# Optimization experiments

Hardware: AMD Instinct MI355X
Metric: run time of the kernel (lower is better)

## Reference

```python
import jax, jax.numpy as jnp
import numpy as np

NUM_HEADS = 16
ROPE_THETA = 10000.0


def _rope_angles(seq_len, head_dim, dtype):
    # lucidrains rotary_embedding_torch: freqs = theta^(-2i/d) for i in 0..d/2,
    # angles = pos * freq, then each angle repeated twice along last dim (interleaved pairs).
    inv_freq = 1.0 / (ROPE_THETA ** (jnp.arange(0, head_dim, 2, dtype=jnp.float32) / head_dim))
    angles = jnp.arange(seq_len, dtype=jnp.float32)[:, None] * inv_freq  # [N, D/2]
    return jnp.repeat(angles, 2, axis=-1).astype(dtype)  # [N, D]


def _rotate_half(t):
    # interleaved pairs: (x0, x1) -> (-x1, x0)
    t1 = t[..., ::2]
    t2 = t[..., 1::2]
    return jnp.stack([-t2, t1], axis=-1).reshape(t.shape)


def _apply_rope(t, cos, sin):
    # t: [B, H, N, D]; cos/sin: [N, D]
    return t * cos + _rotate_half(t) * sin


def setup_inputs() -> dict:
    key = jax.random.key(0)
    ks = jax.random.split(key, 5)
    B, N, C = 4, 1024, 1024
    return {
        "x": jax.random.normal(ks[0], (B, N, C), dtype=jnp.float32),
        "w_qkv": jax.random.normal(ks[1], (C, 3 * C), dtype=jnp.float32) * (C ** -0.5),
        "b_qkv": jax.random.normal(ks[2], (3 * C,), dtype=jnp.float32) * 0.02,
        "w_proj": jax.random.normal(ks[3], (C, C), dtype=jnp.float32) * (C ** -0.5),
        "b_proj": jax.random.normal(ks[4], (C,), dtype=jnp.float32) * 0.02,
    }


def reference(x, w_qkv, b_qkv, w_proj, b_proj):
    B, N, C = x.shape
    H = NUM_HEADS
    D = C // H

    qkv = x @ w_qkv + b_qkv  # [B, N, 3C]
    qkv = qkv.reshape(B, N, 3, H, D).transpose(2, 0, 3, 1, 4)  # [3, B, H, N, D]
    q, k, v = qkv[0], qkv[1], qkv[2]

    ang = _rope_angles(N, D, x.dtype)
    cos, sin = jnp.cos(ang), jnp.sin(ang)
    q = _apply_rope(q, cos, sin)
    k = _apply_rope(k, cos, sin)

    scale = D ** -0.5  # SDPA default scale
    scores = jnp.einsum("bhqd,bhkd->bhqk", q, k) * scale
    attn = jax.nn.softmax(scores, axis=-1)
    out = jnp.einsum("bhqk,bhkd->bhqd", attn, v)  # [B, H, N, D]

    out = out.transpose(0, 2, 1, 3).reshape(B, N, C)
    return out @ w_proj + b_proj
```

## Files before the change

### kernel.cpp

```cpp
#include <hip/hip_runtime.h>
#include <math.h>

#define BB 4
#define NN 1024
#define CC 1024
#define HH 16
#define DD 64
#define N3 3072

typedef __attribute__((ext_vector_type(8))) short bf16x8;
typedef __attribute__((ext_vector_type(8))) _Float16 f16x8;
typedef __attribute__((ext_vector_type(4))) _Float16 f16x4;
typedef __attribute__((ext_vector_type(4))) float f32x4;
typedef __attribute__((ext_vector_type(4))) unsigned int u32x4;

struct ushort4_t { unsigned short x, y, z, w; };

static __device__ __forceinline__ unsigned short f2b(float f) {
    union { float f; unsigned int u; } v; v.f = f;
    unsigned int r = (v.u + 0x7fffu + ((v.u >> 16) & 1u)) >> 16;
    return (unsigned short)r;
}

static __device__ __forceinline__ void ldg_lds16(const void* g, void* l) {
    __builtin_amdgcn_global_load_lds(
        (const __attribute__((address_space(1))) unsigned int*)g,
        (__attribute__((address_space(3))) unsigned int*)l, 16, 0, 0);
}

__global__ __launch_bounds__(256) void prep(const float* __restrict__ x,
                                            const float* __restrict__ wq,
                                            const float* __restrict__ wp,
                                            _Float16* __restrict__ Xh,
                                            _Float16* __restrict__ Wqt,
                                            _Float16* __restrict__ Wpt,
                                            float* __restrict__ ct,
                                            float* __restrict__ st) {
    const int blk = blockIdx.x;
    const int t = threadIdx.x;
    if (blk < 4096) {
        int tid = blk * 256 + t;
        float4 v = ((const float4*)x)[tid];
        f16x4 o = {(_Float16)v.x, (_Float16)v.y, (_Float16)v.z, (_Float16)v.w};
        ((f16x4*)Xh)[tid] = o;
    } else if (blk < 5632) {
        int idx = blk - 4096;
        int n  = (idx % 12) * 256 + t;
        int k0 = (idx / 12) * 8;
        f16x8 o;
        #pragma unroll
        for (int kk = 0; kk < 8; kk++)
            o[kk] = (_Float16)wq[(size_t)(k0 + kk) * N3 + n];
        *(f16x8*)(Wqt + (size_t)n * 1024 + k0) = o;
    } else if (blk < 6144) {
        int idx = blk - 5632;
        int n  = (idx % 4) * 256 + t;
        int k0 = (idx / 4) * 8;
        f16x8 o;
        #pragma unroll
        for (int kk = 0; kk < 8; kk++)
            o[kk] = (_Float16)wp[(size_t)(k0 + kk) * 1024 + n];
        *(f16x8*)(Wpt + (size_t)n * 1024 + k0) = o;
    } else {
        int tid = (blk - 6144) * 256 + t;
        int n = tid >> 5, i = tid & 31;
        double ang = (double)n * exp2(-(double)i * (13.287712379549449 / 32.0));
        ct[tid] = (float)cos(ang);
        st[tid] = (float)sin(ang);
    }
}

static __device__ __forceinline__ void gemm_body_pipe(const char* gA, const char* gB,
                                                      int m0, int n0,
                                                      _Float16* As0, _Float16* As1,
                                                      _Float16* Bs0, _Float16* Bs1,
                                                      int tid, int ln, int qd,
                                                      int wm, int wn, f32x4 acc[4][4]) {
    const int lrow   = tid >> 3;
    const int lchunk = tid & 7;
    const int swz    = (lchunk ^ (lrow & 7)) * 8;

    u32x4 pa[4], pb[4];

    #pragma unroll
    for (int c = 0; c < 4; c++) {
        size_t ra = (size_t)(m0 + c * 32 + lrow) * 2048 + lchunk * 16;
        size_t rb = (size_t)(n0 + c * 32 + lrow) * 2048 + lchunk * 16;
        pa[c] = *(const u32x4*)(gA + ra);
        pb[c] = *(const u32x4*)(gB + rb);
    }
    #pragma unroll
    for (int c = 0; c < 4; c++) {
        *(u32x4*)&As0[(c * 32 + lrow) * 64 + swz] = pa[c];
        *(u32x4*)&Bs0[(c * 32 + lrow) * 64 + swz] = pb[c];
    }
    #pragma unroll
    for (int c = 0; c < 4; c++) {
        size_t ra = (size_t)(m0 + c * 32 + lrow) * 2048 + 128 + lchunk * 16;
        size_t rb = (size_t)(n0 + c * 32 + lrow) * 2048 + 128 + lchunk * 16;
        pa[c] = *(const u32x4*)(gA + ra);
        pb[c] = *(const u32x4*)(gB + rb);
    }
    __syncthreads();

    #pragma unroll
    for (int t = 0; t < 16; t++) {
        const _Float16* Ac = (t & 1) ? As1 : As0;
        const _Float16* Bc = (t & 1) ? Bs1 : Bs0;

        #pragma unroll
        for (int kc = 0; kc < 2; kc++) {
            f16x8 af[4], bf[4];
            #pragma unroll
            for (int i = 0; i < 4; i++)
                af[i] = *(const f16x8*)&Ac[(wm + i * 16 + ln) * 64 +
                                           (((kc * 4 + qd) ^ (ln & 7)) * 8)];
            #pragma unroll
            for (int j = 0; j < 4; j++)
                bf[j] = *(const f16x8*)&Bc[(wn + j * 16 + ln) * 64 +
                                           (((kc * 4 + qd) ^ (ln & 7)) * 8)];
            #pragma unroll
            for (int i = 0; i < 4; i++)
                #pragma unroll
                for (int j = 0; j < 4; j++)
                    acc[i][j] = __builtin_amdgcn_mfma_f32_16x16x32_f16(af[i], bf[j],
                                                                       acc[i][j], 0, 0, 0);
        }

        if (t < 15) {
            _Float16* An = (t & 1) ? As0 : As1;
            _Float16* Bn = (t & 1) ? Bs0 : Bs1;
            #pragma unroll
            for (int c = 0; c < 4; c++) {
                *(u32x4*)&An[(c * 32 + lrow) * 64 + swz] = pa[c];
                *(u32x4*)&Bn[(c * 32 + lrow) * 64 + swz] = pb[c];
            }
            if (t < 14) {
                size_t ko = (size_t)(t + 2) * 128;
                #pragma unroll
                for (int c = 0; c < 4; c++) {
                    size_t ra = (size_t)(m0 + c * 32 + lrow) * 2048 + ko + lchunk * 16;
                    size_t rb = (size_t)(n0 + c * 32 + lrow) * 2048 + ko + lchunk * 16;
                    pa[c] = *(const u32x4*)(gA + ra);
                    pb[c] = *(const u32x4*)(gB + rb);
                }
            }
        }
        __syncthreads();
    }
}

static __device__ __forceinline__ void gemm_body_pipe_n64(const char* gA, const char* gB,
                                                          int m0, int n0,
                                                          _Float16* As0, _Float16* As1,
                                                          _Float16* Bs0, _Float16* Bs1,
                                                          int tid, int ln, int qd,
                                                          int wm, int wn, f32x4 acc[4][2]) {
    const int lrow   = tid >> 3;
    const int lchunk = tid & 7;
    const int swz    = (lchunk ^ (lrow & 7)) * 8;

    u32x4 pa[4], pb[2];

    #pragma unroll
    for (int c = 0; c < 4; c++)
        pa[c] = *(const u32x4*)(gA + (size_t)(m0 + c * 32 + lrow) * 2048 + lchunk * 16);
    #pragma unroll
    for (int c = 0; c < 2; c++)
        pb[c] = *(const u32x4*)(gB + (size_t)(n0 + c * 32 + lrow) * 2048 + lchunk * 16);
    #pragma unroll
    for (int c = 0; c < 4; c++)
        *(u32x4*)&As0[(c * 32 + lrow) * 64 + swz] = pa[c];
    #pragma unroll
    for (int c = 0; c < 2; c++)
        *(u32x4*)&Bs0[(c * 32 + lrow) * 64 + swz] = pb[c];
    #pragma unroll
    for (int c = 0; c < 4; c++)
        pa[c] = *(const u32x4*)(gA + (size_t)(m0 + c * 32 + lrow) * 2048 + 128 + lchunk * 16);
    #pragma unroll
    for (int c = 0; c < 2; c++)
        pb[c] = *(const u32x4*)(gB + (size_t)(n0 + c * 32 + lrow) * 2048 + 128 + lchunk * 16);
    __syncthreads();

    #pragma unroll
    for (int t = 0; t < 16; t++) {
        const _Float16* Ac = (t & 1) ? As1 : As0;
        const _Float16* Bc = (t & 1) ? Bs1 : Bs0;

        #pragma unroll
        for (int kc = 0; kc < 2; kc++) {
            f16x8 af[4], bf[2];
            #pragma unroll
            for (int i = 0; i < 4; i++)
                af[i] = *(const f16x8*)&Ac[(wm + i * 16 + ln) * 64 +
                                           (((kc * 4 + qd) ^ (ln & 7)) * 8)];
            #pragma unroll
            for (int j = 0; j < 2; j++)
                bf[j] = *(const f16x8*)&Bc[(wn + j * 16 + ln) * 64 +
                                           (((kc * 4 + qd) ^ (ln & 7)) * 8)];
            #pragma unroll
            for (int i = 0; i < 4; i++)
                #pragma unroll
                for (int j = 0; j < 2; j++)
                    acc[i][j] = __builtin_amdgcn_mfma_f32_16x16x32_f16(af[i], bf[j],
                                                                       acc[i][j], 0, 0, 0);
        }

        if (t < 15) {
            _Float16* An = (t & 1) ? As0 : As1;
            _Float16* Bn = (t & 1) ? Bs0 : Bs1;
            #pragma unroll
            for (int c = 0; c < 4; c++)
                *(u32x4*)&An[(c * 32 + lrow) * 64 + swz] = pa[c];
            #pragma unroll
            for (int c = 0; c < 2; c++)
                *(u32x4*)&Bn[(c * 32 + lrow) * 64 + swz] = pb[c];
            if (t < 14) {
                size_t ko = (size_t)(t + 2) * 128;
                #pragma unroll
                for (int c = 0; c < 4; c++)
                    pa[c] = *(const u32x4*)(gA + (size_t)(m0 + c * 32 + lrow) * 2048 + ko + lchunk * 16);
                #pragma unroll
                for (int c = 0; c < 2; c++)
                    pb[c] = *(const u32x4*)(gB + (size_t)(n0 + c * 32 + lrow) * 2048 + ko + lchunk * 16);
            }
        }
        __syncthreads();
    }
}

__global__ __launch_bounds__(256) void qkv_mfma(const _Float16* __restrict__ Ah,
                                                const _Float16* __restrict__ Bt,
                                                const float* __restrict__ bias,
                                                const float* __restrict__ cost,
                                                const float* __restrict__ sint,
                                                unsigned short* __restrict__ Q,
                                                unsigned short* __restrict__ K,
                                                unsigned short* __restrict__ Vtg) {
    __shared__ __align__(16) _Float16 As[2][128 * 64];
    __shared__ __align__(16) _Float16 Bs[2][128 * 64];
    const int t = threadIdx.x;
    const int lane = t & 63;
    const int w = t >> 6;
    const int ln = lane & 15, qd = lane >> 4;
    const int n0 = blockIdx.x * 128;
    const int m0 = blockIdx.y * 128;
    const int wm = (w >> 1) * 64, wn = (w & 1) * 64;

    f32x4 acc[4][4];
    #pragma unroll
    for (int i = 0; i < 4; i++)
        #pragma unroll
        for (int j = 0; j < 4; j++) acc[i][j] = (f32x4){0.f, 0.f, 0.f, 0.f};

    gemm_body_pipe((const char*)Ah, (const char*)Bt, m0, n0,
                   As[0], As[1], Bs[0], Bs[1], t, ln, qd, wm, wn, acc);

    const int s = n0 >> 10;
    const int h = ((n0 + wn) >> 6) & 15;
    if (s < 2) {
        unsigned short* dst = (s == 0) ? Q : K;
        const float sc0 = (s == 0) ? 0.125f : 1.0f;
        #pragma unroll
        for (int i = 0; i < 4; i++) {
            #pragma unroll
            for (int reg = 0; reg < 4; reg++) {
                int row = m0 + wm + i * 16 + qd * 4 + reg;
                int b = row >> 10, n = row & 1023;
                size_t obase = (((size_t)(b * HH + h)) * NN + n) * DD;
                #pragma unroll
                for (int j = 0; j < 4; j++) {
                    int d = j * 16 + ln;
                    float v = acc[i][j][reg] + bias[n0 + wn + d];
                    float pv = __shfl_xor(v, 1);
                    float cs = cost[n * 32 + (d >> 1)];
                    float sn = sint[n * 32 + (d >> 1)];
                    float outv = ((d & 1) ? (v * cs + pv * sn) : (v * cs - pv * sn)) * sc0;
                    dst[obase + d] = f2b(outv);
                }
            }
        }
    } else {
        #pragma unroll
        for (int i = 0; i < 4; i++) {
            int row0 = m0 + wm + i * 16 + qd * 4;
            int b = row0 >> 10, n = row0 & 1023;
            size_t tbase = ((size_t)(b * HH + h)) * DD * NN + n;
            #pragma unroll
            for (int j = 0; j < 4; j++) {
                int d = j * 16 + ln;
                float bb = bias[n0 + wn + d];
                ushort4_t pk;
                pk.x = f2b(acc[i][j][0] + bb);
                pk.y = f2b(acc[i][j][1] + bb);
                pk.z = f2b(acc[i][j][2] + bb);
                pk.w = f2b(acc[i][j][3] + bb);
                *(ushort4_t*)&Vtg[tbase + (size_t)d * NN] = pk;
            }
        }
    }
}

__global__ __launch_bounds__(256) void attn_flash(const unsigned short* __restrict__ Qb,
                                                  const unsigned short* __restrict__ Kb,
                                                  const unsigned short* __restrict__ Vtg,
                                                  _Float16* __restrict__ AO) {
    __shared__ __align__(16) unsigned short Ks[3][64 * 64];
    __shared__ __align__(16) unsigned short Vt[2][64 * 64];
    __shared__ __align__(16) unsigned short Ps[4][32 * 64];

    const int t    = threadIdx.x;
    const int lane = t & 63;
    const int w    = t >> 6;
    const int ln   = lane & 15;
    const int qd   = lane >> 4;
    const int bq   = blockIdx.x;
    const int h    = blockIdx.y;
    const int b    = blockIdx.z;
    const size_t base = (size_t)(b * HH + h) * NN * DD;
    const char* Kc = (const char*)(Kb + base);
    const char* Vc = (const char*)(Vtg + base);
    const int xorc = ((lane & 7) ^ (lane >> 3)) * 16;
    const int r8   = lane >> 3;
    const int wrow = w * 16;

    bf16x8 qf[2][2];
    #pragma unroll
    for (int g = 0; g < 2; g++) {
        const unsigned short* qp = Qb + base +
            (size_t)(bq * 128 + w * 32 + g * 16 + ln) * DD + qd * 8;
        qf[g][0] = *(const bf16x8*)qp;
        qf[g][1] = *(const bf16x8*)(qp + 32);
    }

    f32x4 o[2][5];
    #pragma unroll
    for (int g = 0; g < 2; g++)
        #pragma unroll
        for (int x = 0; x < 5; x++) o[g][x] = (f32x4){0.f, 0.f, 0.f, 0.f};

    bf16x8 onesf;
    #pragma unroll
    for (int x = 0; x < 8; x++) onesf[x] = (short)0x3F80;

    #pragma unroll
    for (int tile = 0; tile < 3; tile++)
        #pragma unroll
        for (int c = 0; c < 2; c++) {
            int rr = wrow + c * 8 + r8;
            ldg_lds16(Kc + (size_t)(tile * 64 + rr) * 128 + xorc,
                      &Ks[tile][(wrow + c * 8) * 64]);
        }
    #pragma unroll
    for (int tile = 0; tile < 2; tile++)
        #pragma unroll
        for (int c = 0; c < 2; c++) {
            int rr = wrow + c * 8 + r8;
            ldg_lds16(Vc + (size_t)rr * 2048 + (size_t)tile * 128 + xorc,
                      &Vt[tile][(wrow + c * 8) * 64]);
        }
    __syncthreads();

    f32x4 scur[2][4];
    {
        const unsigned short* KsB = Ks[0];
        #pragma unroll
        for (int j = 0; j < 4; j++) {
            bf16x8 k0f = *(const bf16x8*)&KsB[(ln + 16 * j) * 64 + ((qd ^ (ln & 7)) * 8)];
            bf16x8 k1f = *(const bf16x8*)&KsB[(ln + 16 * j) * 64 + (((4 + qd) ^ (ln & 7)) * 8)];
            #pragma unroll
            for (int g = 0; g < 2; g++) {
                f32x4 sj = {0.f, 0.f, 0.f, 0.f};
                sj = __builtin_amdgcn_mfma_f32_16x16x32_bf16(qf[g][0], k0f, sj, 0, 0, 0);
                sj = __builtin_amdgcn_mfma_f32_16x16x32_bf16(qf[g][1], k1f, sj, 0, 0, 0);
                scur[g][j] = sj;
            }
        }
    }

    const float C1 = 1.44269504f;
    const float C0 = -16.0f * 1.44269504f;

    #pragma unroll
    for (int tt = 0; tt < 16; tt++) {
        f32x4 snext[2][4];
        if (tt < 15) {
            const unsigned short* KsB = Ks[(tt + 1) % 3];
            #pragma unroll
            for (int j = 0; j < 4; j++) {
                bf16x8 k0f = *(const bf16x8*)&KsB[(ln + 16 * j) * 64 + ((qd ^ (ln & 7)) * 8)];
                bf16x8 k1f = *(const bf16x8*)&KsB[(ln + 16 * j) * 64 + (((4 + qd) ^ (ln & 7)) * 8)];
                #pragma unroll
                for (int g = 0; g < 2; g++) {
                    f32x4 sj = {0.f, 0.f, 0.f, 0.f};
                    sj = __builtin_amdgcn_mfma_f32_16x16x32_bf16(qf[g][0], k0f, sj, 0, 0, 0);
                    sj = __builtin_amdgcn_mfma_f32_16x16x32_bf16(qf[g][1], k1f, sj, 0, 0, 0);
                    snext[g][j] = sj;
                }
            }
        }

        unsigned short* PsB = &Ps[w][0];
        #pragma unroll
        for (int g = 0; g < 2; g++)
            #pragma unroll
            for (int j = 0; j < 4; j++)
                #pragma unroll
                for (int r = 0; r < 4; r++) {
                    float p = exp2f(fmaf(scur[g][j][r], C1, C0));
                    union { float f; unsigned int u; } cv; cv.f = p;
                    int m = g * 16 + qd * 4 + r;
                    PsB[m * 64 + ((((ln >> 3) + 2 * j) ^ (m & 7)) * 8) + (ln & 7)] =
                        (unsigned short)((cv.u + 0x8000u) >> 16);
                }

        {
            const unsigned short* VtB = Vt[tt & 1];
            bf16x8 pf[2][2];
            #pragma unroll
            for (int g = 0; g < 2; g++) {
                pf[g][0] = *(const bf16x8*)&PsB[(g * 16 + ln) * 64 + ((qd ^ (ln & 7)) * 8)];
                pf[g][1] = *(const bf16x8*)&PsB[(g * 16 + ln) * 64 + (((4 + qd) ^ (ln & 7)) * 8)];
            }
            #pragma unroll
            for (int j = 0; j < 4; j++) {
                bf16x8 v0f = *(const bf16x8*)&VtB[(ln + 16 * j) * 64 + ((qd ^ (ln & 7)) * 8)];
                bf16x8 v1f = *(const bf16x8*)&VtB[(ln + 16 * j) * 64 + (((4 + qd) ^ (ln & 7)) * 8)];
                #pragma unroll
                for (int g = 0; g < 2; g++) {
                    o[g][j] = __builtin_amdgcn_mfma_f32_16x16x32_bf16(pf[g][0], v0f, o[g][j], 0, 0, 0);
                    o[g][j] = __builtin_amdgcn_mfma_f32_16x16x32_bf16(pf[g][1], v1f, o[g][j], 0, 0, 0);
                }
            }
            #pragma unroll
            for (int g = 0; g < 2; g++) {
                o[g][4] = __builtin_amdgcn_mfma_f32_16x16x32_bf16(pf[g][0], onesf, o[g][4], 0, 0, 0);
                o[g][4] = __builtin_amdgcn_mfma_f32_16x16x32_bf16(pf[g][1], onesf, o[g][4], 0, 0, 0);
            }
        }

        __syncthreads();

        if (tt <= 12) {
            int tile = tt + 3;
            #pragma unroll
            for (int c = 0; c < 2; c++) {
                int rr = wrow + c * 8 + r8;
                ldg_lds16(Kc + (size_t)(tile * 64 + rr) * 128 + xorc,
                          &Ks[tt % 3][(wrow + c * 8) * 64]);
            }
        }
        if (tt <= 13) {
            int tile = tt + 2;
            #pragma unroll
            for (int c = 0; c < 2; c++) {
                int rr = wrow + c * 8 + r8;
                ldg_lds16(Vc + (size_t)rr * 2048 + (size_t)tile * 128 + xorc,
                          &Vt[tt & 1][(wrow + c * 8) * 64]);
            }
        }

        #pragma unroll
        for (int g = 0; g < 2; g++)
            #pragma unroll
            for (int j = 0; j < 4; j++) scur[g][j] = snext[g][j];
    }

    #pragma unroll
    for (int g = 0; g < 2; g++)
        #pragma unroll
        for (int r = 0; r < 4; r++) {
            float inv = 1.0f / o[g][4][r];
            int q = bq * 128 + w * 32 + g * 16 + qd * 4 + r;
            _Float16* op = AO + (((size_t)b * NN + q) * HH + h) * DD + ln;
            op[0]  = (_Float16)(o[g][0][r] * inv);
            op[16] = (_Float16)(o[g][1][r] * inv);
            op[32] = (_Float16)(o[g][2][r] * inv);
            op[48] = (_Float16)(o[g][3][r] * inv);
        }
}

__global__ __launch_bounds__(256) void proj_mfma(const _Float16* __restrict__ Ah,
                                                 const _Float16* __restrict__ Bt,
                                                 const float* __restrict__ bias,
                                                 float* __restrict__ out) {
    __shared__ __align__(16) _Float16 As[2][128 * 64];
    __shared__ __align__(16) _Float16 Bs[2][64 * 64];
    const int t = threadIdx.x;
    const int lane = t & 63;
    const int w = t >> 6;
    const int ln = lane & 15, qd = lane >> 4;
    const int n0 = blockIdx.x * 64;
    const int m0 = blockIdx.y * 128;
    const int wm = (w >> 1) * 64, wn = (w & 1) * 32;

    f32x4 acc[4][2];
    #pragma unroll
    for (int i = 0; i < 4; i++)
        #pragma unroll
        for (int j = 0; j < 2; j++) acc[i][j] = (f32x4){0.f, 0.f, 0.f, 0.f};

    gemm_body_pipe_n64((const char*)Ah, (const char*)Bt, m0, n0,
                       As[0], As[1], Bs[0], Bs[1], t, ln, qd, wm, wn, acc);

    #pragma unroll
    for (int i = 0; i < 4; i++) {
        #pragma unroll
        for (int reg = 0; reg < 4; reg++) {
            int row = m0 + wm + i * 16 + qd * 4 + reg;
            #pragma unroll
            for (int j = 0; j < 2; j++) {
                int col = n0 + wn + j * 16 + ln;
                out[(size_t)row * 1024 + col] = acc[i][j][reg] + bias[col];
            }
        }
    }
}

extern "C" void kernel_launch(void* const* d_in, const int* in_sizes, int n_in,
                              void* d_out, int out_size, void* d_ws, size_t ws_size,
                              hipStream_t stream) {
    const float* x      = (const float*)d_in[0];
    const float* w_qkv  = (const float*)d_in[1];
    const float* b_qkv  = (const float*)d_in[2];
    const float* w_proj = (const float*)d_in[3];
    const float* b_proj = (const float*)d_in[4];
    float* out = (float*)d_out;

    char* ws = (char*)d_ws;
    _Float16* Xh   = (_Float16*)(ws);
    _Float16* Wqt  = (_Float16*)(ws + (8u << 20));
    _Float16* Wpt  = (_Float16*)(ws + (14u << 20));
    unsigned short* Q  = (unsigned short*)(ws + (16u << 20));
    unsigned short* K  = (unsigned short*)(ws + (24u << 20));
    unsigned short* Vt = (unsigned short*)(ws + (32u << 20));
    _Float16* AOh  = (_Float16*)(ws + (40u << 20));
    float* cost    = (float*)(ws + (48u << 20));
    float* sint    = (float*)(ws + (48u << 20) + (128u << 10));

    prep<<<6272, 256, 0, stream>>>(x, w_qkv, w_proj, Xh, Wqt, Wpt, cost, sint);
    qkv_mfma<<<dim3(24, 32), 256, 0, stream>>>(Xh, Wqt, b_qkv, cost, sint, Q, K, Vt);
    attn_flash<<<dim3(8, 16, 4), 256, 0, stream>>>(Q, K, Vt, AOh);
    proj_mfma<<<dim3(16, 32), 256, 0, stream>>>(AOh, Wpt, b_proj, out);
}
```

Measured before the change: 176.0 us.

## Tile weight transpose via LDS, shrink QKV GEMM K-tile, swap attention MFMA operands

The prep kernel now transposes and converts the weight matrices through a 64x64 shared-memory tile, so both the global reads and the writes are coalesced instead of strided. The QKV GEMM uses a templated body with a K-tile of 32 in place of 64, which halves shared memory per block and requests three blocks per SM via launch bounds, in exchange for twice as many barrier iterations. In attention, the QK^T MFMA operands are swapped so each lane holds a transposed score fragment, which lets the probabilities be packed with hardware v_cvt_pk_bf16_f32 and written as 8-byte stores rather than scattered 2-byte stores. The rounding changes from an add-0x8000 trick to the hardware conversion.

```diff
diff --git a/kernel.cpp b/kernel.cpp
--- a/kernel.cpp
+++ b/kernel.cpp
@@ -13,6 +13,7 @@
 typedef __attribute__((ext_vector_type(4))) _Float16 f16x4;
 typedef __attribute__((ext_vector_type(4))) float f32x4;
 typedef __attribute__((ext_vector_type(4))) unsigned int u32x4;
+typedef __attribute__((ext_vector_type(2))) unsigned int u32x2;
 
 struct ushort4_t { unsigned short x, y, z, w; };
 
@@ -36,6 +37,7 @@
                                             _Float16* __restrict__ Wpt,
                                             float* __restrict__ ct,
                                             float* __restrict__ st) {
+    __shared__ __align__(16) _Float16 T[64][72];
     const int blk = blockIdx.x;
     const int t = threadIdx.x;
     if (blk < 4096) {
@@ -43,26 +45,48 @@
         float4 v = ((const float4*)x)[tid];
         f16x4 o = {(_Float16)v.x, (_Float16)v.y, (_Float16)v.z, (_Float16)v.w};
         ((f16x4*)Xh)[tid] = o;
-    } else if (blk < 5632) {
-        int idx = blk - 4096;
-        int n  = (idx % 12) * 256 + t;
-        int k0 = (idx / 12) * 8;
-        f16x8 o;
-        #pragma unroll
-        for (int kk = 0; kk < 8; kk++)
-            o[kk] = (_Float16)wq[(size_t)(k0 + kk) * N3 + n];
-        *(f16x8*)(Wqt + (size_t)n * 1024 + k0) = o;
-    } else if (blk < 6144) {
-        int idx = blk - 5632;
-        int n  = (idx % 4) * 256 + t;
-        int k0 = (idx / 4) * 8;
-        f16x8 o;
-        #pragma unroll
-        for (int kk = 0; kk < 8; kk++)
-            o[kk] = (_Float16)wp[(size_t)(k0 + kk) * 1024 + n];
-        *(f16x8*)(Wpt + (size_t)n * 1024 + k0) = o;
+    } else if (blk < 5120) {
+        const float* src; _Float16* dst; int ns, k0, n0;
+        if (blk < 4864) {
+            int idx = blk - 4096;
+            k0 = (idx & 15) * 64; n0 = (idx >> 4) * 64;
+            src = wq; dst = Wqt; ns = N3;
+        } else {
+            int idx = blk - 4864;
+            k0 = (idx & 15) * 64; n0 = (idx >> 4) * 64;
+            src = wp; dst = Wpt; ns = 1024;
+        }
+        {
+            const int r  = t >> 2;
+            const int cf = (t & 3) * 16;
+            const float* sp = src + (size_t)(k0 + r) * ns + n0 + cf;
+            float4 v0 = *(const float4*)(sp);
+            float4 v1 = *(const float4*)(sp + 4);
+            float4 v2 = *(const float4*)(sp + 8);
+            float4 v3 = *(const float4*)(sp + 12);
+            f16x8 a, b;
+            a[0]=(_Float16)v0.x; a[1]=(_Float16)v0.y; a[2]=(_Float16)v0.z; a[3]=(_Float16)v0.w;
+            a[4]=(_Float16)v1.x; a[5]=(_Float16)v1.y; a[6]=(_Float16)v1.z; a[7]=(_Float16)v1.w;
+            b[0]=(_Float16)v2.x; b[1]=(_Float16)v2.y; b[2]=(_Float16)v2.z; b[3]=(_Float16)v2.w;
+            b[4]=(_Float16)v3.x; b[5]=(_Float16)v3.y; b[6]=(_Float16)v3.z; b[7]=(_Float16)v3.w;
+            *(f16x8*)&T[r][cf]     = a;
+            *(f16x8*)&T[r][cf + 8] = b;
+        }
+        __syncthreads();
+        {
+            const int n  = t >> 2;
+            const int kc = t & 3;
+            f16x8 o0, o1;
+            #pragma unroll
+            for (int kk = 0; kk < 8; kk++) o0[kk] = T[kc * 16 + kk][n];
+            #pragma unroll
+            for (int kk = 0; kk < 8; kk++) o1[kk] = T[kc * 16 + 8 + kk][n];
+            _Float16* dp = dst + (size_t)(n0 + n) * 1024 + k0 + kc * 16;
+            *(f16x8*)dp       = o0;
+            *(f16x8*)(dp + 8) = o1;
+        }
     } else {
-        int tid = (blk - 6144) * 256 + t;
+        int tid = (blk - 5120) * 256 + t;
         int n = tid >> 5, i = tid & 31;
         double ang = (double)n * exp2(-(double)i * (13.287712379549449 / 32.0));
         ct[tid] = (float)cos(ang);
@@ -70,80 +94,74 @@
     }
 }
 
-static __device__ __forceinline__ void gemm_body_pipe(const char* gA, const char* gB,
-                                                      int m0, int n0,
-                                                      _Float16* As0, _Float16* As1,
-                                                      _Float16* Bs0, _Float16* Bs1,
-                                                      int tid, int ln, int qd,
-                                                      int wm, int wn, f32x4 acc[4][4]) {
-    const int lrow   = tid >> 3;
-    const int lchunk = tid & 7;
-    const int swz    = (lchunk ^ (lrow & 7)) * 8;
-
-    u32x4 pa[4], pb[4];
-
-    #pragma unroll
-    for (int c = 0; c < 4; c++) {
-        size_t ra = (size_t)(m0 + c * 32 + lrow) * 2048 + lchunk * 16;
-        size_t rb = (size_t)(n0 + c * 32 + lrow) * 2048 + lchunk * 16;
-        pa[c] = *(const u32x4*)(gA + ra);
-        pb[c] = *(const u32x4*)(gB + rb);
-    }
-    #pragma unroll
-    for (int c = 0; c < 4; c++) {
-        *(u32x4*)&As0[(c * 32 + lrow) * 64 + swz] = pa[c];
-        *(u32x4*)&Bs0[(c * 32 + lrow) * 64 + swz] = pb[c];
-    }
-    #pragma unroll
-    for (int c = 0; c < 4; c++) {
-        size_t ra = (size_t)(m0 + c * 32 + lrow) * 2048 + 128 + lchunk * 16;
-        size_t rb = (size_t)(n0 + c * 32 + lrow) * 2048 + 128 + lchunk * 16;
-        pa[c] = *(const u32x4*)(gA + ra);
-        pb[c] = *(const u32x4*)(gB + rb);
-    }
+template<int BM, int BN>
+static __device__ __forceinline__ void gemm_body32(const char* gA, const char* gB,
+                                                   int m0, int n0,
+                                                   _Float16* As0, _Float16* As1,
+                                                   _Float16* Bs0, _Float16* Bs1,
+                                                   int tid, int ln, int qd,
+                                                   int wm, int wn,
+                                                   f32x4 (&acc)[BM / 32][BN / 32]) {
+    constexpr int PA = BM / 64, PB = BN / 64, MR = BM / 32, NR = BN / 32;
+    const int lrow = tid >> 2;
+    const int lc   = tid & 3;
+    const int swz  = (lc ^ (lrow & 3)) * 8;
+    const int rsz  = (qd ^ (ln & 3)) * 8;
+
+    u32x4 pa[PA], pb[PB];
+
+    #pragma unroll
+    for (int p = 0; p < PA; p++)
+        pa[p] = *(const u32x4*)(gA + (size_t)(m0 + p * 64 + lrow) * 2048 + lc * 16);
+    #pragma unroll
+    for (int p = 0; p < PB; p++)
+        pb[p] = *(const u32x4*)(gB + (size_t)(n0 + p * 64 + lrow) * 2048 + lc * 16);
+    #pragma unroll
+    for (int p = 0; p < PA; p++) *(u32x4*)&As0[(p * 64 + lrow) * 32 + swz] = pa[p];
+    #pragma unroll
+    for (int p = 0; p < PB; p++) *(u32x4*)&Bs0[(p * 64 + lrow) * 32 + swz] = pb[p];
+    #pragma unroll
+    for (int p = 0; p < PA; p++)
+        pa[p] = *(const u32x4*)(gA + (size_t)(m0 + p * 64 + lrow) * 2048 + 64 + lc * 16);
+    #pragma unroll
+    for (int p = 0; p < PB; p++)
+        pb[p] = *(const u32x4*)(gB + (size_t)(n0 + p * 64 + lrow) * 2048 + 64 + lc * 16);
     __syncthreads();
 
     #pragma unroll
-    for (int t = 0; t < 16; t++) {
+    for (int t = 0; t < 32; t++) {
         const _Float16* Ac = (t & 1) ? As1 : As0;
         const _Float16* Bc = (t & 1) ? Bs1 : Bs0;
 
-        #pragma unroll
-        for (int kc = 0; kc < 2; kc++) {
-            f16x8 af[4], bf[4];
-            #pragma unroll
-            for (int i = 0; i < 4; i++)
-                af[i] = *(const f16x8*)&Ac[(wm + i * 16 + ln) * 64 +
-                                           (((kc * 4 + qd) ^ (ln & 7)) * 8)];
-            #pragma unroll
-            for (int j = 0; j < 4; j++)
-                bf[j] = *(const f16x8*)&Bc[(wn + j * 16 + ln) * 64 +
-                                           (((kc * 4 + qd) ^ (ln & 7)) * 8)];
-            #pragma unroll
-            for (int i = 0; i < 4; i++)
-                #pragma unroll
-                for (int j = 0; j < 4; j++)
-                    acc[i][j] = __builtin_amdgcn_mfma_f32_16x16x32_f16(af[i], bf[j],
-                                                                       acc[i][j], 0, 0, 0);
-        }
-
-        if (t < 15) {
+        f16x8 af[MR], bf[NR];
+        #pragma unroll
+        for (int i = 0; i < MR; i++)
+            af[i] = *(const f16x8*)&Ac[(wm + i * 16 + ln) * 32 + rsz];
+        #pragma unroll
+        for (int j = 0; j < NR; j++)
+            bf[j] = *(const f16x8*)&Bc[(wn + j * 16 + ln) * 32 + rsz];
+        #pragma unroll
+        for (int i = 0; i < MR; i++)
+            #pragma unroll
+            for (int j = 0; j < NR; j++)
+                acc[i][j] = __builtin_amdgcn_mfma_f32_16x16x32_f16(af[i], bf[j],
+                                                                   acc[i][j], 0, 0, 0);
+
+        if (t < 31) {
             _Float16* An = (t & 1) ? As0 : As1;
             _Float16* Bn = (t & 1) ? Bs0 : Bs1;
             #pragma unroll
-            for (int c = 0; c < 4; c++) {
-                *(u32x4*)&An[(c * 32 + lrow) * 64 + swz] = pa[c];
-                *(u32x4*)&Bn[(c * 32 + lrow) * 64 + swz] = pb[c];
-            }
-            if (t < 14) {
-                size_t ko = (size_t)(t + 2) * 128;
-                #pragma unroll
-                for (int c = 0; c < 4; c++) {
-                    size_t ra = (size_t)(m0 + c * 32 + lrow) * 2048 + ko + lchunk * 16;
-                    size_t rb = (size_t)(n0 + c * 32 + lrow) * 2048 + ko + lchunk * 16;
-                    pa[c] = *(const u32x4*)(gA + ra);
-                    pb[c] = *(const u32x4*)(gB + rb);
-                }
+            for (int p = 0; p < PA; p++) *(u32x4*)&An[(p * 64 + lrow) * 32 + swz] = pa[p];
+            #pragma unroll
+            for (int p = 0; p < PB; p++) *(u32x4*)&Bn[(p * 64 + lrow) * 32 + swz] = pb[p];
+            if (t < 30) {
+                size_t ko = (size_t)(t + 2) * 64;
+                #pragma unroll
+                for (int p = 0; p < PA; p++)
+                    pa[p] = *(const u32x4*)(gA + (size_t)(m0 + p * 64 + lrow) * 2048 + ko + lc * 16);
+                #pragma unroll
+                for (int p = 0; p < PB; p++)
+                    pb[p] = *(const u32x4*)(gB + (size_t)(n0 + p * 64 + lrow) * 2048 + ko + lc * 16);
             }
         }
         __syncthreads();
@@ -229,16 +247,16 @@
     }
 }
 
-__global__ __launch_bounds__(256) void qkv_mfma(const _Float16* __restrict__ Ah,
-                                                const _Float16* __restrict__ Bt,
-                                                const float* __restrict__ bias,
-                                                const float* __restrict__ cost,
-                                                const float* __restrict__ sint,
-                                                unsigned short* __restrict__ Q,
-                                                unsigned short* __restrict__ K,
-                                                unsigned short* __restrict__ Vtg) {
-    __shared__ __align__(16) _Float16 As[2][128 * 64];
-    __shared__ __align__(16) _Float16 Bs[2][128 * 64];
+__global__ __launch_bounds__(256, 3) void qkv_mfma(const _Float16* __restrict__ Ah,
+                                                   const _Float16* __restrict__ Bt,
+                                                   const float* __restrict__ bias,
+                                                   const float* __restrict__ cost,
+                                                   const float* __restrict__ sint,
+                                                   unsigned short* __restrict__ Q,
+                                                   unsigned short* __restrict__ K,
+                                                   unsigned short* __restrict__ Vtg) {
+    __shared__ __align__(16) _Float16 As[2][128 * 32];
+    __shared__ __align__(16) _Float16 Bs[2][128 * 32];
     const int t = threadIdx.x;
     const int lane = t & 63;
     const int w = t >> 6;
@@ -253,8 +271,8 @@
         #pragma unroll
         for (int j = 0; j < 4; j++) acc[i][j] = (f32x4){0.f, 0.f, 0.f, 0.f};
 
-    gemm_body_pipe((const char*)Ah, (const char*)Bt, m0, n0,
-                   As[0], As[1], Bs[0], Bs[1], t, ln, qd, wm, wn, acc);
+    gemm_body32<128, 128>((const char*)Ah, (const char*)Bt, m0, n0,
+                          As[0], As[1], Bs[0], Bs[1], t, ln, qd, wm, wn, acc);
 
     const int s = n0 >> 10;
     const int h = ((n0 + wn) >> 6) & 15;
@@ -371,8 +389,8 @@
             #pragma unroll
             for (int g = 0; g < 2; g++) {
                 f32x4 sj = {0.f, 0.f, 0.f, 0.f};
-                sj = __builtin_amdgcn_mfma_f32_16x16x32_bf16(qf[g][0], k0f, sj, 0, 0, 0);
-                sj = __builtin_amdgcn_mfma_f32_16x16x32_bf16(qf[g][1], k1f, sj, 0, 0, 0);
+                sj = __builtin_amdgcn_mfma_f32_16x16x32_bf16(k0f, qf[g][0], sj, 0, 0, 0);
+                sj = __builtin_amdgcn_mfma_f32_16x16x32_bf16(k1f, qf[g][1], sj, 0, 0, 0);
                 scur[g][j] = sj;
             }
         }
@@ -380,6 +398,7 @@
 
     const float C1 = 1.44269504f;
     const float C0 = -16.0f * 1.44269504f;
+    const int swp = 2 * (ln & 7);
 
     #pragma unroll
     for (int tt = 0; tt < 16; tt++) {
@@ -393,8 +412,8 @@
                 #pragma unroll
                 for (int g = 0; g < 2; g++) {
                     f32x4 sj = {0.f, 0.f, 0.f, 0.f};
-                    sj = __builtin_amdgcn_mfma_f32_16x16x32_bf16(qf[g][0], k0f, sj, 0, 0, 0);
-                    sj = __builtin_amdgcn_mfma_f32_16x16x32_bf16(qf[g][1], k1f, sj, 0, 0, 0);
+                    sj = __builtin_amdgcn_mfma_f32_16x16x32_bf16(k0f, qf[g][0], sj, 0, 0, 0);
+                    sj = __builtin_amdgcn_mfma_f32_16x16x32_bf16(k1f, qf[g][1], sj, 0, 0, 0);
                     snext[g][j] = sj;
                 }
             }
@@ -402,17 +421,21 @@
 
         unsigned short* PsB = &Ps[w][0];
         #pragma unroll
-        for (int g = 0; g < 2; g++)
-            #pragma unroll
-            for (int j = 0; j < 4; j++)
-                #pragma unroll
-                for (int r = 0; r < 4; r++) {
-                    float p = exp2f(fmaf(scur[g][j][r], C1, C0));
-                    union { float f; unsigned int u; } cv; cv.f = p;
-                    int m = g * 16 + qd * 4 + r;
-                    PsB[m * 64 + ((((ln >> 3) + 2 * j) ^ (m & 7)) * 8) + (ln & 7)] =
-                        (unsigned short)((cv.u + 0x8000u) >> 16);
-                }
+        for (int g = 0; g < 2; g++) {
+            char* rowp = (char*)PsB + (g * 16 + ln) * 128;
+            #pragma unroll
+            for (int j = 0; j < 4; j++) {
+                float p0 = exp2f(fmaf(scur[g][j][0], C1, C0));
+                float p1 = exp2f(fmaf(scur[g][j][1], C1, C0));
+                float p2 = exp2f(fmaf(scur[g][j][2], C1, C0));
+                float p3 = exp2f(fmaf(scur[g][j][3], C1, C0));
+                unsigned int lo, hi;
+                asm("v_cvt_pk_bf16_f32 %0, %1, %2" : "=v"(lo) : "v"(p0), "v"(p1));
+                asm("v_cvt_pk_bf16_f32 %0, %1, %2" : "=v"(hi) : "v"(p2), "v"(p3));
+                u32x2 pk; pk[0] = lo; pk[1] = hi;
+                *(u32x2*)(rowp + (((4 * j + qd) ^ swp) * 8)) = pk;
+            }
+        }
 
         {
             const unsigned short* VtB = Vt[tt & 1];
@@ -538,7 +561,7 @@
     float* cost    = (float*)(ws + (48u << 20));
     float* sint    = (float*)(ws + (48u << 20) + (128u << 10));
 
-    prep<<<6272, 256, 0, stream>>>(x, w_qkv, w_proj, Xh, Wqt, Wpt, cost, sint);
+    prep<<<5248, 256, 0, stream>>>(x, w_qkv, w_proj, Xh, Wqt, Wpt, cost, sint);
     qkv_mfma<<<dim3(24, 32), 256, 0, stream>>>(Xh, Wqt, b_qkv, cost, sint, Q, K, Vt);
     attn_flash<<<dim3(8, 16, 4), 256, 0, stream>>>(Q, K, Vt, AOh);
     proj_mfma<<<dim3(16, 32), 256, 0, stream>>>(AOh, Wpt, b_proj, out);
```

Measured after the change: 178.8 us. No clear change (+1.6%).
